# Optimization experiments

Hardware: AMD Instinct MI355X
Metric: run time of the kernel (lower is better)

## Reference

```python
import jax, jax.numpy as jnp
import numpy as np

THRESHOLD = 0.0

def setup_inputs() -> dict:
    key = jax.random.key(0)
    k1, k2 = jax.random.split(key)
    B, N, D = 16384, 16384, 128
    query_embeddings = jax.random.normal(k1, (B, D), dtype=jnp.float32)
    # module normalizes learned centroids; emulate for provided centroids too-faithfulness
    # NOTE: forward itself does NOT normalize provided cluster_embeddings, so we pass raw randn
    cluster_embeddings = jax.random.normal(k2, (N, D), dtype=jnp.float32)
    return {"query_embeddings": query_embeddings,
            "cluster_embeddings": cluster_embeddings,
            "top_k": 8}

def reference(query_embeddings, cluster_embeddings, top_k):
    # cosine similarity path: plain matmul (B, N)
    all_similarities = jnp.matmul(query_embeddings, cluster_embeddings.T)
    k = min(int(top_k), all_similarities.shape[1])
    top_k_similarities, top_k_indices = jax.lax.top_k(all_similarities, k)
    mask = top_k_similarities >= THRESHOLD
    cluster_ids = jnp.where(mask, top_k_indices, -1)
    return (cluster_ids, top_k_similarities, all_similarities)
```

## Files before the change

### kernel.cpp

```cpp
#include <hip/hip_runtime.h>
#include <math.h>

#define NROWS 16384
#define NCOLS 16384
#define DIM   128
#define TM    64
#define TN    64
#define NSPLIT 4
#define CPS   (NCOLS/NSPLIT)
#define NCH   (CPS/TN)
#define KP    16

typedef __attribute__((ext_vector_type(8))) short bf16x8;
typedef __attribute__((ext_vector_type(4))) float f32x4;

__device__ __forceinline__ unsigned short bf16_rne(float x) {
  unsigned u = __float_as_uint(x);
  unsigned r = u + 0x7fffu + ((u >> 16) & 1u);
  return (unsigned short)(r >> 16);
}

__device__ __forceinline__ unsigned mkkey(float v, int col) {
  unsigned b = __float_as_uint(v);
  unsigned u = b ^ (unsigned)(((int)b >> 31) | (int)0x80000000);
  return (u & 0xFFFFC000u) | (unsigned)(16383 - col);
}

#define INSERT(tk, key) do {                                                  \
  unsigned _k = (key);                                                        \
  if (_k > tk[KP - 1]) {                                                      \
    tk[KP - 1] = _k;                                                          \
    _Pragma("unroll")                                                         \
    for (int _m = KP - 1; _m > 0; --_m) {                                     \
      unsigned _hi = tk[_m - 1] > tk[_m] ? tk[_m - 1] : tk[_m];               \
      unsigned _lo = tk[_m - 1] > tk[_m] ? tk[_m] : tk[_m - 1];               \
      tk[_m - 1] = _hi; tk[_m] = _lo;                                         \
    }                                                                         \
  }                                                                           \
} while (0)

#define BAR() do {                                   \
  __builtin_amdgcn_sched_barrier(0);                 \
  asm volatile("s_waitcnt lgkmcnt(0)" ::: "memory"); \
  __builtin_amdgcn_s_barrier();                      \
  __builtin_amdgcn_sched_barrier(0);                 \
} while (0)

__global__ __launch_bounds__(256) void split_kernel(
    const float* __restrict__ C, unsigned char* __restrict__ Cimg)
{
  const unsigned u = blockIdx.x * 256 + threadIdx.x;
  const int c  = u & 16383;
  const int kk = u >> 14;
  const f32x4* src = (const f32x4*)(C + (size_t)c * DIM + kk * 16);
  f32x4 f[4];
  f[0] = src[0]; f[1] = src[1]; f[2] = src[2]; f[3] = src[3];
  const unsigned chunkbase = ((unsigned)(c >> 6)) << 14;
  const unsigned T = ((((unsigned)c >> 4) & 3u) << 2) | ((unsigned)kk >> 1);
  #pragma unroll
  for (int s = 0; s < 2; ++s) {
    bf16x8 h;
    #pragma unroll
    for (int e = 0; e < 8; ++e)
      h[e] = (short)bf16_rne(f[s * 2 + (e >> 2)][e & 3]);
    unsigned ln = (unsigned)(c & 15) | ((((unsigned)kk * 2 + s) & 3u) << 4);
    *(bf16x8*)&Cimg[chunkbase + (T << 10) + (ln << 4)] = h;
  }
}

__global__ __launch_bounds__(256, 4) void sim_topk_kernel(
    const float* __restrict__ Q, const unsigned char* __restrict__ Cimg,
    float* __restrict__ S, int* __restrict__ cand)
{
  __shared__ __align__(16) unsigned char lds[32768];
  const int t = threadIdx.x;
  const int w = t >> 6, lane = t & 63;

  const int bid = blockIdx.x;
  const int xcd = bid & 7;
  const int cs  = xcd >> 1;
  const int rb  = ((xcd & 1) << 7) | (bid >> 3);
  const int row0 = rb * TM;
  const int col0 = cs * CPS;
  const int phase = rb & (NCH - 1);

  const int arow = row0 + w * 16 + (lane & 15);
  bf16x8 a_h[4];
  {
    const f32x4* Qp = (const f32x4*)(Q + (size_t)arow * DIM) + (lane >> 4) * 2;
    #pragma unroll
    for (int ks = 0; ks < 4; ++ks) {
      f32x4 x0 = Qp[ks * 8], x1 = Qp[ks * 8 + 1];
      #pragma unroll
      for (int e = 0; e < 8; ++e)
        a_h[ks][e] = (short)bf16_rne((e < 4) ? x0[e & 3] : x1[e & 3]);
    }
  }

  f32x4 st[4];
  auto gload = [&](int ch) {
    const f32x4* p = (const f32x4*)(Cimg + (((size_t)(cs * NCH + ch)) << 14)) + t;
    st[0] = p[0]; st[1] = p[256]; st[2] = p[512]; st[3] = p[768];
  };
  auto swrite = [&](unsigned buf) {
    #pragma unroll
    for (int r = 0; r < 4; ++r)
      *(f32x4*)&lds[buf + (unsigned)r * 4096u + (unsigned)t * 16u] = st[r];
  };

  gload(phase); swrite(0u); gload((phase + 1) & (NCH - 1));
  BAR();

  unsigned tk[KP];
  #pragma unroll
  for (int j = 0; j < KP; ++j) tk[j] = 0u;

  for (int i = 0; i < NCH; ++i) {
    const int ch = (phase + i) & (NCH - 1);
    const unsigned cur = (i & 1) ? 16384u : 0u;

    if (i + 1 < NCH) swrite(cur ^ 16384u);
    if (i + 2 < NCH) gload((phase + i + 2) & (NCH - 1));

    f32x4 acc[4];
    #pragma unroll
    for (int c = 0; c < 4; ++c) acc[c] = {0.f, 0.f, 0.f, 0.f};
    #pragma unroll
    for (int ks = 0; ks < 4; ++ks) {
      #pragma unroll
      for (int ct = 0; ct < 4; ++ct) {
        unsigned o = cur + ((unsigned)(ct * 4 + ks) << 10) + ((unsigned)lane << 4);
        bf16x8 bh = *(const bf16x8*)&lds[o];
        acc[ct] = __builtin_amdgcn_mfma_f32_16x16x32_bf16(bh, a_h[ks], acc[ct], 0, 0, 0);
      }
    }

    {
      const int colg0 = col0 + ch * TN;
      const int cloc  = (lane >> 4) * 4;
      float* sp = &S[(size_t)arow * NCOLS + colg0 + cloc];
      #pragma unroll
      for (int ct = 0; ct < 4; ++ct) {
        *(f32x4*)&sp[ct * 16] = acc[ct];
        const int cg = colg0 + ct * 16 + cloc;
        #pragma unroll
        for (int e = 0; e < 4; ++e)
          INSERT(tk, mkkey(acc[ct][e], cg + e));
      }
    }
    BAR();
  }

  #pragma unroll
  for (int off = 16; off <= 32; off <<= 1) {
    unsigned ov[KP];
    #pragma unroll
    for (int j = 0; j < KP; ++j)
      ov[j] = (unsigned)__shfl_xor((int)tk[j], off);
    #pragma unroll
    for (int j = 0; j < KP; ++j) INSERT(tk, ov[j]);
  }
  if (lane < 16) {
    int* dst = cand + ((size_t)(row0 + w * 16 + lane) * NSPLIT + cs) * KP;
    #pragma unroll
    for (int j = 0; j < KP; ++j) dst[j] = 16383 - (int)(tk[j] & 0x3FFFu);
  }
}

__global__ __launch_bounds__(256) void rerank_kernel(
    const float* __restrict__ Q, const float* __restrict__ C,
    const int* __restrict__ cand, float* __restrict__ out)
{
  const int t = threadIdx.x, w = t >> 6, lane = t & 63;
  const int r = blockIdx.x * 4 + w;
  const f32x4* Q4 = (const f32x4*)(Q + (size_t)r * DIM);

  const int cidx = cand[(size_t)r * (NSPLIT * KP) + lane];
  const f32x4* C4 = (const f32x4*)(C + (size_t)cidx * DIM);

  double acc = 0.0;
  #pragma unroll 8
  for (int d4 = 0; d4 < 32; ++d4) {
    f32x4 q = Q4[d4];
    f32x4 c = C4[d4];
    acc += (double)q[0] * (double)c[0];
    acc += (double)q[1] * (double)c[1];
    acc += (double)q[2] * (double)c[2];
    acc += (double)q[3] * (double)c[3];
  }

  double mv = acc;
  int    mi = cidx;

  float* oi = out;
  float* os = out + (size_t)NROWS * 8;

  for (int k = 0; k < 8; ++k) {
    double bv = mv; int bi = mi;
    #pragma unroll
    for (int off = 32; off >= 1; off >>= 1) {
      double ov = __shfl_xor(bv, off);
      int    o2 = __shfl_xor(bi, off);
      if (ov > bv || (ov == bv && o2 < bi)) { bv = ov; bi = o2; }
    }
    if (lane == 0) {
      os[(size_t)r * 8 + k] = (float)bv;
      oi[(size_t)r * 8 + k] = (bv >= 0.0) ? (float)bi : -1.0f;
    }
    if (mi == bi) mv = -1.0e300;
  }
}

extern "C" void kernel_launch(void* const* d_in, const int* in_sizes, int n_in,
                              void* d_out, int out_size, void* d_ws, size_t ws_size,
                              hipStream_t stream) {
  const float* Q = (const float*)d_in[0];
  const float* C = (const float*)d_in[1];
  float* out = (float*)d_out;
  float* S   = out + (size_t)2 * NROWS * 8;

  unsigned char* Cimg = (unsigned char*)d_ws;
  int* cand = (int*)(Cimg + 4194304);

  split_kernel<<<dim3(512), dim3(256), 0, stream>>>(C, Cimg);
  sim_topk_kernel<<<dim3((NROWS / TM) * NSPLIT), dim3(256), 0, stream>>>(Q, Cimg, S, cand);
  rerank_kernel<<<dim3(NROWS / 4), dim3(256), 0, stream>>>(Q, C, cand, out);
}
```

Measured before the change: 503.5 us.

## Stage similarity tiles in LDS bounce buffer for coalesced row-contiguous stores

Each wave now writes its MFMA accumulator tiles into a per-wave swizzled LDS bounce buffer. Every four column chunks it flushes 256 contiguous floats per row to S, so full 1KB row segments are written instead of scattered 16-byte pieces. To make room it drops the LDS double buffer for a single buffer with two barriers per iteration, raises LDS to 80KB, lowers the occupancy hint to 2 blocks per CU, and aligns the chunk phase to multiples of four. This trades load/compute overlap and occupancy for better write coalescing on the large S output.

```diff
diff --git a/kernel.cpp b/kernel.cpp
--- a/kernel.cpp
+++ b/kernel.cpp
@@ -68,11 +68,11 @@
   }
 }
 
-__global__ __launch_bounds__(256, 4) void sim_topk_kernel(
+__global__ __launch_bounds__(256, 2) void sim_topk_kernel(
     const float* __restrict__ Q, const unsigned char* __restrict__ Cimg,
     float* __restrict__ S, int* __restrict__ cand)
 {
-  __shared__ __align__(16) unsigned char lds[32768];
+  __shared__ __align__(16) unsigned char lds[81920];
   const int t = threadIdx.x;
   const int w = t >> 6, lane = t & 63;
 
@@ -82,7 +82,8 @@
   const int rb  = ((xcd & 1) << 7) | (bid >> 3);
   const int row0 = rb * TM;
   const int col0 = cs * CPS;
-  const int phase = rb & (NCH - 1);
+  const int phase = (rb & 15) << 2;
+  unsigned char* bounce = lds + 16384u + (unsigned)w * 16384u;
 
   const int arow = row0 + w * 16 + (lane & 15);
   bf16x8 a_h[4];
@@ -102,25 +103,28 @@
     const f32x4* p = (const f32x4*)(Cimg + (((size_t)(cs * NCH + ch)) << 14)) + t;
     st[0] = p[0]; st[1] = p[256]; st[2] = p[512]; st[3] = p[768];
   };
-  auto swrite = [&](unsigned buf) {
+  auto swrite = [&]() {
     #pragma unroll
     for (int r = 0; r < 4; ++r)
-      *(f32x4*)&lds[buf + (unsigned)r * 4096u + (unsigned)t * 16u] = st[r];
+      *(f32x4*)&lds[(unsigned)r * 4096u + (unsigned)t * 16u] = st[r];
   };
 
-  gload(phase); swrite(0u); gload((phase + 1) & (NCH - 1));
-  BAR();
+  gload(phase);
 
   unsigned tk[KP];
   #pragma unroll
   for (int j = 0; j < KP; ++j) tk[j] = 0u;
 
+  const int r16 = lane & 15;
+  const unsigned rsw = (unsigned)(r16 & 7);
+
   for (int i = 0; i < NCH; ++i) {
     const int ch = (phase + i) & (NCH - 1);
-    const unsigned cur = (i & 1) ? 16384u : 0u;
-
-    if (i + 1 < NCH) swrite(cur ^ 16384u);
-    if (i + 2 < NCH) gload((phase + i + 2) & (NCH - 1));
+
+    BAR();
+    swrite();
+    if (i + 1 < NCH) gload((phase + i + 1) & (NCH - 1));
+    BAR();
 
     f32x4 acc[4];
     #pragma unroll
@@ -129,7 +133,7 @@
     for (int ks = 0; ks < 4; ++ks) {
       #pragma unroll
       for (int ct = 0; ct < 4; ++ct) {
-        unsigned o = cur + ((unsigned)(ct * 4 + ks) << 10) + ((unsigned)lane << 4);
+        unsigned o = ((unsigned)(ct * 4 + ks) << 10) + ((unsigned)lane << 4);
         bf16x8 bh = *(const bf16x8*)&lds[o];
         acc[ct] = __builtin_amdgcn_mfma_f32_16x16x32_bf16(bh, a_h[ks], acc[ct], 0, 0, 0);
       }
@@ -137,18 +141,26 @@
 
     {
       const int colg0 = col0 + ch * TN;
-      const int cloc  = (lane >> 4) * 4;
-      float* sp = &S[(size_t)arow * NCOLS + colg0 + cloc];
       #pragma unroll
       for (int ct = 0; ct < 4; ++ct) {
-        *(f32x4*)&sp[ct * 16] = acc[ct];
-        const int cg = colg0 + ct * 16 + cloc;
+        unsigned X = (unsigned)((ch & 3) * 16 + ct * 4 + (lane >> 4));
+        *(f32x4*)&bounce[(unsigned)r16 * 1024u + ((X ^ rsw) << 4)] = acc[ct];
+        const int cg = colg0 + ct * 16 + (lane >> 4) * 4;
         #pragma unroll
         for (int e = 0; e < 4; ++e)
           INSERT(tk, mkkey(acc[ct][e], cg + e));
       }
     }
-    BAR();
+
+    if ((i & 3) == 3) {
+      const int gbase = col0 + (ch & ~3) * TN;
+      #pragma unroll
+      for (int r = 0; r < 16; ++r) {
+        f32x4 v = *(const f32x4*)&bounce[(unsigned)r * 1024u +
+                      (((unsigned)(lane ^ (r & 7))) << 4)];
+        *(f32x4*)&S[(size_t)(row0 + w * 16 + r) * NCOLS + gbase + lane * 4] = v;
+      }
+    }
   }
 
   #pragma unroll
```

Result: no change. 508.1 us (+0.9%).
